# Optimization experiments

Hardware: AMD Instinct MI355X
Metric: run time of the kernel (lower is better)

Reference implementation:

```python
import jax, jax.numpy as jnp
import numpy as np

B, T, V, E, H, K, PAD = 32, 512, 50000, 256, 512, 17, 0


def setup_inputs() -> dict:
    key = jax.random.key(0)
    ks = jax.random.split(key, 16)
    s = 0.05
    input_ids = jax.random.randint(ks[0], (B, T), 1, V)
    lengths = jax.random.randint(ks[1], (B,), T // 2, T + 1)  # >=1 token, mask[:,0] all True
    tags = jax.random.randint(ks[2], (B, T), 0, K)
    mask = jnp.arange(T)[None, :] < lengths[:, None]
    emb = (jax.random.normal(ks[3], (V, E)) * s).at[PAD].set(0.0)  # padding_idx row zeroed
    w_ih_f = jax.random.normal(ks[4], (4 * H, E)) * s
    w_hh_f = jax.random.normal(ks[5], (4 * H, H)) * s
    b_f = jax.random.normal(ks[6], (4 * H,)) * s
    w_ih_b = jax.random.normal(ks[7], (4 * H, E)) * s
    w_hh_b = jax.random.normal(ks[8], (4 * H, H)) * s
    b_b = jax.random.normal(ks[9], (4 * H,)) * s
    w_cls = jax.random.normal(ks[10], (K, 2 * H)) * s
    b_cls = jax.random.normal(ks[11], (K,)) * s
    start_trans = jax.random.normal(ks[12], (K,)) * s
    trans = jax.random.normal(ks[13], (K, K)) * s
    end_trans = jax.random.normal(ks[14], (K,)) * s
    return dict(input_ids=input_ids, lengths=lengths, tags=tags, mask=mask,
                emb=emb, w_ih_f=w_ih_f, w_hh_f=w_hh_f, b_f=b_f,
                w_ih_b=w_ih_b, w_hh_b=w_hh_b, b_b=b_b,
                w_cls=w_cls, b_cls=b_cls,
                start_trans=start_trans, trans=trans, end_trans=end_trans)


def _lstm(xg, w_hh):
    # xg: [B,T,4H] = x @ W_ih^T + b (precomputed); scan adds recurrent term.
    Bq, Hq = xg.shape[0], w_hh.shape[1]

    def step(carry, g_in):
        h, c = carry
        g = g_in + h @ w_hh.T
        i, f, gg, o = jnp.split(g, 4, axis=-1)  # torch gate order i,f,g,o
        c = jax.nn.sigmoid(f) * c + jax.nn.sigmoid(i) * jnp.tanh(gg)
        h = jax.nn.sigmoid(o) * jnp.tanh(c)
        return (h, c), h

    init = (jnp.zeros((Bq, Hq), xg.dtype), jnp.zeros((Bq, Hq), xg.dtype))
    _, hs = jax.lax.scan(step, init, jnp.swapaxes(xg, 0, 1))
    return jnp.swapaxes(hs, 0, 1)  # [B,T,H]


def _forward_math(input_ids, lengths, tags, mask, emb,
                  w_ih_f, w_hh_f, b_f, w_ih_b, w_hh_b, b_b,
                  w_cls, b_cls, start_trans, trans, end_trans):
    x = emb[input_ids]  # [B,T,E]
    # forward direction over padded seq (valid prefix is causally correct)
    hf = _lstm(x @ w_ih_f.T + b_f, w_hh_f)
    # backward direction: reverse each sequence within its own length (packed semantics)
    t = jnp.arange(input_ids.shape[1])[None, :]
    rev = jnp.where(t < lengths[:, None], lengths[:, None] - 1 - t, t)  # involution on valid region
    xr = jnp.take_along_axis(x, rev[:, :, None], axis=1)
    hb = _lstm(xr @ w_ih_b.T + b_b, w_hh_b)
    hb = jnp.take_along_axis(hb, rev[:, :, None], axis=1)
    enc = jnp.concatenate([hf, hb], axis=-1)  # dropout = identity (eval / p=0)
    emissions = enc @ w_cls.T + b_cls  # [B,T,K]
    m = mask.astype(emissions.dtype)
    # ---- CRF numerator (gold path score) ----
    emis_sc = jnp.sum(jnp.take_along_axis(emissions, tags[:, :, None], axis=2)[..., 0] * m, axis=1)
    tr_sc = jnp.sum(trans[tags[:, :-1], tags[:, 1:]] * m[:, 1:], axis=1)
    last_tag = jnp.take_along_axis(tags, (lengths - 1)[:, None], axis=1)[:, 0]
    numer = start_trans[tags[:, 0]] + emis_sc + tr_sc + end_trans[last_tag]
    # ---- CRF partition (forward algorithm) ----
    def fstep(alpha, inp):
        e_t, m_t = inp
        nxt = jax.nn.logsumexp(alpha[:, :, None] + trans[None, :, :] + e_t[:, None, :], axis=1)
        return jnp.where(m_t[:, None], nxt, alpha), None

    alpha0 = start_trans[None, :] + emissions[:, 0]
    alphaT, _ = jax.lax.scan(
        fstep, alpha0,
        (jnp.swapaxes(emissions[:, 1:], 0, 1), jnp.swapaxes(mask[:, 1:], 0, 1)))
    logZ = jax.nn.logsumexp(alphaT + end_trans[None, :], axis=1)
    return -jnp.mean(numer - logZ)  # reduction='mean', negated


def reference(input_ids, lengths, tags, mask, emb, w_ih_f, w_hh_f, b_f,
              w_ih_b, w_hh_b, b_b, w_cls, b_cls, start_trans, trans, end_trans):
    return _forward_math(input_ids, lengths, tags, mask, emb, w_ih_f, w_hh_f, b_f,
                         w_ih_b, w_hh_b, b_b, w_cls, b_cls, start_trans, trans, end_trans)
```

## Files before the change

kernel.cpp:

```cpp
#include <hip/hip_runtime.h>
#include <hip/hip_bf16.h>
#include <stdint.h>

#define B_  32
#define T_  512
#define E_  256
#define H_  512
#define K_  17

typedef unsigned short us;
typedef __attribute__((ext_vector_type(8))) short short8;
typedef __attribute__((ext_vector_type(4))) float f32x4;

__device__ __forceinline__ float bf2f(unsigned int u16) {
    union { unsigned int i; float f; } v; v.i = u16 << 16; return v.f;
}
__device__ __forceinline__ us f2bf(float f) {
    union { float f; unsigned int i; } v; v.f = f;
    unsigned int b = v.i;
    return (us)((b + 0x7FFFu + ((b >> 16) & 1u)) >> 16);
}
__device__ __forceinline__ float sigf(float x) { return 1.0f / (1.0f + __expf(-x)); }
__device__ __forceinline__ float tanhf_(float x) { return 1.0f - 2.0f / (__expf(2.0f * x) + 1.0f); }

__global__ void k_cvt(const float* __restrict__ src, us* __restrict__ dst, int n4) {
    int i = blockIdx.x * 256 + threadIdx.x;
    if (i < n4) {
        float4 v = ((const float4*)src)[i];
        uint2 p;
        p.x = (uint32_t)f2bf(v.x) | ((uint32_t)f2bf(v.y) << 16);
        p.y = (uint32_t)f2bf(v.z) | ((uint32_t)f2bf(v.w) << 16);
        ((uint2*)dst)[i] = p;
    }
}

__global__ void k_init(const int* __restrict__ ids, const int* __restrict__ lengths,
                       int* __restrict__ ids2, int* __restrict__ marker,
                       int* __restrict__ flags, float* __restrict__ out) {
    int idx = blockIdx.x * 256 + threadIdx.x;
    if (idx == 0) { *marker = 1; out[0] = -3328.0f; }
    if (idx < 1024) flags[idx] = 0;
    if (idx < 2 * B_ * T_) {
        int dir = idx >> 14;
        int r   = idx & 16383;
        int t   = r >> 5;
        int b   = r & 31;
        int l   = lengths[b];
        int tt  = (dir == 0) ? t : ((t < l) ? (l - 1 - t) : t);
        ids2[idx] = ids[b * T_ + tt];
    }
}

__launch_bounds__(256)
__global__ void k_xg(const us* __restrict__ emb,
                     const us* __restrict__ wf, const float* __restrict__ bfv,
                     const us* __restrict__ wb, const float* __restrict__ bbv,
                     const int* __restrict__ ids2, us* __restrict__ xg,
                     int* __restrict__ marker) {
    if (blockIdx.x == 0 && blockIdx.y == 0 && blockIdx.z == 0 && threadIdx.x == 0)
        atomicOr(marker, 2);
    int mt = blockIdx.x, nt = blockIdx.y, dir = blockIdx.z;
    const us* W      = dir ? wb  : wf;
    const float* bias = dir ? bbv : bfv;
    const int* id2 = ids2 + dir * (B_ * T_);
    us* xgd = xg + (size_t)dir * B_ * T_ * 2048;
    int m0 = mt * 64, n0 = nt * 64;
    __shared__ __align__(16) us As[64][136];
    __shared__ __align__(16) us Bs[64][136];
    int tid = threadIdx.x;
    int wv = tid >> 6, lane = tid & 63;
    int lm = lane & 15, lg = lane >> 4;
    f32x4 z = {0.f, 0.f, 0.f, 0.f};
    f32x4 acc[4] = {z, z, z, z};
    for (int half = 0; half < 2; ++half) {
        for (int c = tid; c < 1024; c += 256) {
            int row = c >> 4, cb = c & 15;
            int mg = m0 + row;
            int j = mg >> 2, g = mg & 3;
            *(uint4*)&As[row][cb * 8] =
                *(const uint4*)(W + ((size_t)(g * H_ + j)) * E_ + half * 128 + cb * 8);
            int gi = id2[n0 + row];
            *(uint4*)&Bs[row][cb * 8] =
                *(const uint4*)(emb + (size_t)gi * E_ + half * 128 + cb * 8);
        }
        __syncthreads();
#pragma unroll
        for (int kt = 0; kt < 4; ++kt) {
            short8 a = *(const short8*)&As[wv * 16 + lm][kt * 32 + lg * 8];
#pragma unroll
            for (int n2 = 0; n2 < 4; ++n2) {
                short8 b = *(const short8*)&Bs[n2 * 16 + lm][kt * 32 + lg * 8];
                acc[n2] = __builtin_amdgcn_mfma_f32_16x16x32_bf16(a, b, acc[n2], 0, 0, 0);
            }
        }
        __syncthreads();
    }
    int jgb = m0 + wv * 16 + lg * 4;
    int j = jgb >> 2;
#pragma unroll
    for (int n2 = 0; n2 < 4; ++n2) {
        int token = n0 + n2 * 16 + lm;
        us p[4];
#pragma unroll
        for (int q = 0; q < 4; ++q)
            p[q] = f2bf(acc[n2][q] + bias[q * H_ + j]);
        uint2 pv;
        pv.x = (uint32_t)p[0] | ((uint32_t)p[1] << 16);
        pv.y = (uint32_t)p[2] | ((uint32_t)p[3] << 16);
        *(uint2*)(xgd + (size_t)token * 2048 + jgb) = pv;
    }
}

__launch_bounds__(256)
__global__ void k_lstm(const us* __restrict__ whf, const us* __restrict__ whb,
                       const us* __restrict__ xg,
                       us* __restrict__ h_state, us* __restrict__ h_out,
                       int* __restrict__ flags, int* __restrict__ marker) {
    int bid = blockIdx.x;
    int role = bid & 7;
    int tid = threadIdx.x;
    if (bid == 0 && tid == 0) atomicOr(marker, 4);
    if (role >= 2) return;
    int dir = role, w = bid >> 3;
    const us* Wg = dir ? whb : whf;
    __shared__ __align__(16) us Ws[64 * 512];
    __shared__ __align__(4)  us Hx[32 * 16];
    for (int c = tid; c < 4096; c += 256) {
        int row = c >> 6, cb = c & 63;
        int rt = row >> 4, rl = row & 15;
        int jj = rl >> 2, g = rl & 3;
        int srcRow = g * H_ + w * 16 + rt * 4 + jj;
        uint4 v = *(const uint4*)(Wg + (size_t)srcRow * H_ + cb * 8);
        int lb = row * 1024 + ((cb * 16) ^ ((row & 7) << 4));
        *(uint4*)((char*)Ws + lb) = v;
    }
    __syncthreads();
    int wv = tid >> 6, lane = tid & 63;
    int nb = wv & 1, rh = wv >> 1;
    int lm = lane & 15, lg = lane >> 4;
    int b = nb * 16 + lm;
    int jl0 = rh * 8 + lg;
    int jl1 = rh * 8 + 4 + lg;
    const us* xgd = xg + (size_t)dir * B_ * T_ * 2048;
    us* hod = h_out + (size_t)dir * B_ * T_ * H_;
    int* slots = flags + dir * 512;
    const uint64_t* hbase = (const uint64_t*)h_state + (size_t)dir * 8192;
    uint32_t* hw32 = (uint32_t*)h_state + (size_t)dir * 16384;
    float cc0 = 0.f, cc1 = 0.f;
    bool alive = true;
    uint2 vr0 = *(const uint2*)(xgd + ((size_t)b) * 2048 + (w * 16 + jl0) * 4);
    uint2 vr1 = *(const uint2*)(xgd + ((size_t)b) * 2048 + (w * 16 + jl1) * 4);
#pragma unroll 1
    for (int t = 0; t < T_; ++t) {
        f32x4 acc[2];
        if (t > 0) {
            if (wv == 0) {
                int polls = 0;
                for (;;) {
                    int v = (lane < 32)
                        ? __hip_atomic_load(&slots[lane * 16], __ATOMIC_RELAXED, __HIP_MEMORY_SCOPE_AGENT)
                        : 0x7fffffff;
                    if (__all(v >= t) || !alive) break;
                    __builtin_amdgcn_s_sleep(1);
                    if (++polls > 300000) {
                        if (lane == 0) atomicOr(marker, 32);
                        alive = false;
                    }
                }
            }
            __syncthreads();
            const uint64_t* hp = hbase + ((t - 1) & 1) * 4096 + (size_t)b * 128 + lg * 2;
            uint64_t hv[32];
#pragma unroll
            for (int kt = 0; kt < 16; ++kt) {
                hv[2 * kt]     = __hip_atomic_load(hp + kt * 8,     __ATOMIC_RELAXED, __HIP_MEMORY_SCOPE_AGENT);
                hv[2 * kt + 1] = __hip_atomic_load(hp + kt * 8 + 1, __ATOMIC_RELAXED, __HIP_MEMORY_SCOPE_AGENT);
            }
            acc[0][0] = bf2f(vr0.x & 0xffff); acc[0][1] = bf2f(vr0.x >> 16);
            acc[0][2] = bf2f(vr0.y & 0xffff); acc[0][3] = bf2f(vr0.y >> 16);
            acc[1][0] = bf2f(vr1.x & 0xffff); acc[1][1] = bf2f(vr1.x >> 16);
            acc[1][2] = bf2f(vr1.y & 0xffff); acc[1][3] = bf2f(vr1.y >> 16);
#pragma unroll
            for (int ti = 0; ti < 2; ++ti) {
                int r0 = (rh * 2 + ti) * 16 + lm;
                const char* abase = (const char*)Ws + r0 * 1024;
                int sw = (r0 & 7) << 4;
#pragma unroll
                for (int kt = 0; kt < 16; ++kt) {
                    union { uint64_t u[2]; short8 s; } bu;
                    bu.u[0] = hv[2 * kt]; bu.u[1] = hv[2 * kt + 1];
                    short8 a = *(const short8*)(abase + ((kt * 64 + lg * 16) ^ sw));
                    acc[ti] = __builtin_amdgcn_mfma_f32_16x16x32_bf16(a, bu.s, acc[ti], 0, 0, 0);
                }
            }
        } else {
            acc[0][0] = bf2f(vr0.x & 0xffff); acc[0][1] = bf2f(vr0.x >> 16);
            acc[0][2] = bf2f(vr0.y & 0xffff); acc[0][3] = bf2f(vr0.y >> 16);
            acc[1][0] = bf2f(vr1.x & 0xffff); acc[1][1] = bf2f(vr1.x >> 16);
            acc[1][2] = bf2f(vr1.y & 0xffff); acc[1][3] = bf2f(vr1.y >> 16);
        }
        cc0 = sigf(acc[0][1]) * cc0 + sigf(acc[0][0]) * tanhf_(acc[0][2]);
        float h0 = sigf(acc[0][3]) * tanhf_(cc0);
        cc1 = sigf(acc[1][1]) * cc1 + sigf(acc[1][0]) * tanhf_(acc[1][2]);
        float h1 = sigf(acc[1][3]) * tanhf_(cc1);
        us p0 = f2bf(h0), p1 = f2bf(h1);
        Hx[b * 16 + jl0] = p0;
        Hx[b * 16 + jl1] = p1;
        hod[((size_t)b * T_ + t) * H_ + w * 16 + jl0] = p0;
        hod[((size_t)b * T_ + t) * H_ + w * 16 + jl1] = p1;
        __syncthreads();
        {
            uint32_t v = ((const uint32_t*)Hx)[tid];
            int bb = tid >> 3, jp = tid & 7;
            atomicExch(&hw32[(size_t)(t & 1) * 8192 + (size_t)bb * 256 + w * 8 + jp], v);
        }
        __syncthreads();
        if (tid == 0) atomicExch(&slots[w * 16], t + 1);
        if (t + 1 < T_) {
            vr0 = *(const uint2*)(xgd + ((size_t)((t + 1) * 32 + b)) * 2048 + (w * 16 + jl0) * 4);
            vr1 = *(const uint2*)(xgd + ((size_t)((t + 1) * 32 + b)) * 2048 + (w * 16 + jl1) * 4);
        }
    }
}

__launch_bounds__(256)
__global__ void k_emis(const us* __restrict__ h_out,
                       const us* __restrict__ wcls, const float* __restrict__ bcls,
                       const int* __restrict__ lengths, float* __restrict__ emis,
                       int* __restrict__ marker) {
    if (blockIdx.x == 0 && threadIdx.x == 0) atomicOr(marker, 8);
    __shared__ __align__(8) us Wc[17][1032];
    int tid = threadIdx.x;
    for (int c = tid; c < 17 * 256; c += 256) {
        int row = c >> 8; int c4 = (c & 255) * 4;
        *(uint2*)&Wc[row][c4] = *(const uint2*)(wcls + (size_t)row * 1024 + c4);
    }
    __syncthreads();
    int i = blockIdx.x * 8 + (tid >> 5);
    int k = tid & 31;
    int b = i >> 9, t = i & 511;
    int l = lengths[b];
    int trv = (t < l) ? (l - 1 - t) : t;
    const us* hf = h_out + ((size_t)(0 * B_ + b) * T_ + t) * H_;
    const us* hb = h_out + ((size_t)(1 * B_ + b) * T_ + trv) * H_;
    if (k < K_) {
        float acc = bcls[k];
        for (int e = 0; e < H_; e += 4) {
            uint2 hv = *(const uint2*)(hf + e);
            uint2 wv = *(const uint2*)&Wc[k][e];
            acc = fmaf(bf2f(hv.x & 0xffff), bf2f(wv.x & 0xffff), acc);
            acc = fmaf(bf2f(hv.x >> 16),    bf2f(wv.x >> 16),    acc);
            acc = fmaf(bf2f(hv.y & 0xffff), bf2f(wv.y & 0xffff), acc);
            acc = fmaf(bf2f(hv.y >> 16),    bf2f(wv.y >> 16),    acc);
        }
        for (int e = 0; e < H_; e += 4) {
            uint2 hv = *(const uint2*)(hb + e);
            uint2 wv = *(const uint2*)&Wc[k][512 + e];
            acc = fmaf(bf2f(hv.x & 0xffff), bf2f(wv.x & 0xffff), acc);
            acc = fmaf(bf2f(hv.x >> 16),    bf2f(wv.x >> 16),    acc);
            acc = fmaf(bf2f(hv.y & 0xffff), bf2f(wv.y & 0xffff), acc);
            acc = fmaf(bf2f(hv.y >> 16),    bf2f(wv.y >> 16),    acc);
        }
        emis[(size_t)i * 20 + k] = acc;
    }
}

__global__ void k_crf(const float* __restrict__ emis, const int* __restrict__ tags,
                      const int* __restrict__ lengths,
                      const float* __restrict__ start_t, const float* __restrict__ trans_t,
                      const float* __restrict__ end_t, float* __restrict__ res,
                      int* __restrict__ marker) {
    if (blockIdx.x == 0 && threadIdx.x == 0) atomicOr(marker, 16);
    __shared__ float tr[17][18];
    int b = blockIdx.x, tid = threadIdx.x;
    for (int i = tid; i < 289; i += 64) tr[i / 17][i % 17] = trans_t[i];
    __syncthreads();
    int l = lengths[b];
    const int* tg = tags + b * T_;
    const float* eb = emis + (size_t)b * T_ * 20;
    float sn = 0.f;
    for (int t = tid; t < T_; t += 64) {
        if (t < l) {
            sn += eb[t * 20 + tg[t]];
            if (t >= 1) sn += tr[tg[t - 1]][tg[t]];
        }
    }
#pragma unroll
    for (int off = 32; off; off >>= 1) sn += __shfl_xor(sn, off, 64);
    float numer = sn + start_t[tg[0]] + end_t[tg[l - 1]];
    int k = (tid < K_) ? tid : (K_ - 1);
    float trc[17];
#pragma unroll
    for (int j = 0; j < 17; ++j) trc[j] = trans_t[j * 17 + k];
    float alpha = start_t[k] + eb[k];
    for (int t = 1; t < l; ++t) {
        float av[17];
        float m = -1e30f;
#pragma unroll
        for (int j = 0; j < 17; ++j) {
            av[j] = __shfl(alpha, j) + trc[j];
            m = fmaxf(m, av[j]);
        }
        float s = 0.f;
#pragma unroll
        for (int j = 0; j < 17; ++j) s += __expf(av[j] - m);
        alpha = m + __logf(s) + eb[t * 20 + k];
    }
    float v = (tid < K_) ? (alpha + end_t[tid]) : -1e30f;
    float m2 = v;
#pragma unroll
    for (int off = 32; off; off >>= 1) m2 = fmaxf(m2, __shfl_xor(m2, off, 64));
    float s2 = __expf(v - m2);
#pragma unroll
    for (int off = 32; off; off >>= 1) s2 += __shfl_xor(s2, off, 64);
    if (tid == 0) res[b] = numer - (m2 + __logf(s2));
}

__global__ void k_fin(const float* __restrict__ res, int* __restrict__ marker,
                      int hostmask, float* __restrict__ out) {
    int tid = threadIdx.x;
    if (hostmask != 0) {
        if (tid == 0) out[0] = -(16384.0f + 512.0f * (float)hostmask);
        return;
    }
    int dm = atomicOr(marker, 0);
    if (dm != 31) {
        if (tid == 0) out[0] = -(8192.0f + 128.0f * (float)(dm & 63));
        return;
    }
    float v = (tid < B_) ? res[tid] : 0.f;
    unsigned long long nb = __ballot(v != v);
    if (nb != 0ULL) {
        if (tid == 0) out[0] = -(4096.0f + (float)(__ffsll((long long)nb) - 1));
        return;
    }
#pragma unroll
    for (int off = 32; off; off >>= 1) v += __shfl_xor(v, off, 64);
    if (tid == 0) out[0] = -(v / (float)B_);
}

extern "C" void kernel_launch(void* const* d_in, const int* in_sizes, int n_in,
                              void* d_out, int out_size, void* d_ws, size_t ws_size,
                              hipStream_t stream) {
    const int* ids      = (const int*)d_in[0];
    const int* lengths  = (const int*)d_in[1];
    const int* tags     = (const int*)d_in[2];
    const float* emb_f  = (const float*)d_in[4];
    const float* wihf_f = (const float*)d_in[5];
    const float* whhf_f = (const float*)d_in[6];
    const float* bfv    = (const float*)d_in[7];
    const float* wihb_f = (const float*)d_in[8];
    const float* whhb_f = (const float*)d_in[9];
    const float* bbv    = (const float*)d_in[10];
    const float* wcls_f = (const float*)d_in[11];
    const float* bcls   = (const float*)d_in[12];
    const float* start  = (const float*)d_in[13];
    const float* trans  = (const float*)d_in[14];
    const float* endt   = (const float*)d_in[15];
    float* out = (float*)d_out;

    int hm = 0;
    if (n_in != 16 || out_size != 1) hm |= 8;
    const int exp_sz[16] = {
        16384, 32, 16384, 16384,
        12800000,
        524288, 1048576, 2048,
        524288, 1048576, 2048,
        17408, 17,
        17, 289, 17
    };
    if (!(hm & 8))
        for (int i = 0; i < 16; ++i)
            if (in_sizes[i] != exp_sz[i]) hm |= 2;

    char* w = (char*)d_ws;
    size_t off = 0;
    auto carve = [&](size_t bytes) { void* p = w + off; off += (bytes + 255) & ~(size_t)255; return p; };
    int* ids2    = (int*)carve((size_t)2 * B_ * T_ * 4);
    int* marker  = (int*)carve(256);
    int* flags   = (int*)carve(4096);
    float* res   = (float*)carve(256);
    float* emis  = (float*)carve((size_t)B_ * T_ * 20 * 4);
    us* xg       = (us*)carve((size_t)2 * B_ * T_ * 2048 * 2);
    us* h_st     = (us*)carve((size_t)2 * 2 * B_ * H_ * 2);
    us* h_out    = (us*)carve((size_t)2 * B_ * T_ * H_ * 2);
    us* emb_b    = (us*)carve((size_t)12800000 * 2);
    us* wihf_b   = (us*)carve((size_t)524288 * 2);
    us* wihb_b   = (us*)carve((size_t)524288 * 2);
    us* whhf_b   = (us*)carve((size_t)1048576 * 2);
    us* whhb_b   = (us*)carve((size_t)1048576 * 2);
    us* wcls_b   = (us*)carve((size_t)17408 * 2);
    if (off > ws_size) hm |= 4;

    (void)hipGetLastError();
    if ((hm & (2 | 4 | 8)) == 0) {
        k_init<<<(2 * B_ * T_ + 255) / 256, 256, 0, stream>>>(ids, lengths, ids2, marker, flags, out);
        k_cvt<<<(12800000 / 4 + 255) / 256, 256, 0, stream>>>(emb_f,  emb_b,  12800000 / 4);
        k_cvt<<<(524288   / 4 + 255) / 256, 256, 0, stream>>>(wihf_f, wihf_b, 524288 / 4);
        k_cvt<<<(524288   / 4 + 255) / 256, 256, 0, stream>>>(wihb_f, wihb_b, 524288 / 4);
        k_cvt<<<(1048576  / 4 + 255) / 256, 256, 0, stream>>>(whhf_f, whhf_b, 1048576 / 4);
        k_cvt<<<(1048576  / 4 + 255) / 256, 256, 0, stream>>>(whhb_f, whhb_b, 1048576 / 4);
        k_cvt<<<(17408    / 4 + 255) / 256, 256, 0, stream>>>(wcls_f, wcls_b, 17408 / 4);
        k_xg<<<dim3(2048 / 64, B_ * T_ / 64, 2), 256, 0, stream>>>(emb_b, wihf_b, bfv, wihb_b, bbv, ids2, xg, marker);
        k_lstm<<<256, 256, 0, stream>>>(whhf_b, whhb_b, xg, h_st, h_out, flags, marker);
        k_emis<<<B_ * T_ / 8, 256, 0, stream>>>(h_out, wcls_b, bcls, lengths, emis, marker);
        k_crf<<<B_, 64, 0, stream>>>(emis, tags, lengths, start, trans, endt, res, marker);
        if (hipGetLastError() != hipSuccess) hm |= 1;
    }
    k_fin<<<1, 64, 0, stream>>>(res, marker, hm, out);
}
```

Before: 2.890 ms.

## Enlarge xg GEMM tiles and replace LSTM block barrier with per-wave flags

The input-projection GEMM now uses 128x128 tiles, with each wave computing a 4x4 grid of MFMA fragments, to raise data reuse and cut block count. In the recurrent LSTM kernel, each wave now publishes its own ready flag after waiting for its h stores, instead of going through a block-wide barrier and a single thread. Pollers read four flags per lane with 64-bit loads. The h_out stores move after the flag publish so they are off the critical path. This relies on the flag slot spacing (16 ints per w, 4 waves) fitting within each w's region, and on the memory ordering being correct without the barrier.

```diff
diff --git a/kernel.cpp b/kernel.cpp
--- a/kernel.cpp
+++ b/kernel.cpp
@@ -64,16 +64,21 @@
     const float* bias = dir ? bbv : bfv;
     const int* id2 = ids2 + dir * (B_ * T_);
     us* xgd = xg + (size_t)dir * B_ * T_ * 2048;
-    int m0 = mt * 64, n0 = nt * 64;
-    __shared__ __align__(16) us As[64][136];
-    __shared__ __align__(16) us Bs[64][136];
+    int m0 = mt * 128, n0 = nt * 128;
+    __shared__ __align__(16) us As[128][136];
+    __shared__ __align__(16) us Bs[128][136];
     int tid = threadIdx.x;
     int wv = tid >> 6, lane = tid & 63;
+    int wm = wv >> 1, wn = wv & 1;
     int lm = lane & 15, lg = lane >> 4;
     f32x4 z = {0.f, 0.f, 0.f, 0.f};
-    f32x4 acc[4] = {z, z, z, z};
+    f32x4 acc[4][4];
+#pragma unroll
+    for (int i = 0; i < 4; ++i)
+#pragma unroll
+        for (int j = 0; j < 4; ++j) acc[i][j] = z;
     for (int half = 0; half < 2; ++half) {
-        for (int c = tid; c < 1024; c += 256) {
+        for (int c = tid; c < 2048; c += 256) {
             int row = c >> 4, cb = c & 15;
             int mg = m0 + row;
             int j = mg >> 2, g = mg & 3;
@@ -86,28 +91,39 @@
         __syncthreads();
 #pragma unroll
         for (int kt = 0; kt < 4; ++kt) {
-            short8 a = *(const short8*)&As[wv * 16 + lm][kt * 32 + lg * 8];
-#pragma unroll
-            for (int n2 = 0; n2 < 4; ++n2) {
-                short8 b = *(const short8*)&Bs[n2 * 16 + lm][kt * 32 + lg * 8];
-                acc[n2] = __builtin_amdgcn_mfma_f32_16x16x32_bf16(a, b, acc[n2], 0, 0, 0);
+            short8 a[4], b[4];
+#pragma unroll
+            for (int f = 0; f < 4; ++f) {
+                a[f] = *(const short8*)&As[wm * 64 + f * 16 + lm][kt * 32 + lg * 8];
+                b[f] = *(const short8*)&Bs[wn * 64 + f * 16 + lm][kt * 32 + lg * 8];
             }
+#pragma unroll
+            for (int fm = 0; fm < 4; ++fm)
+#pragma unroll
+                for (int fn = 0; fn < 4; ++fn)
+                    acc[fm][fn] = __builtin_amdgcn_mfma_f32_16x16x32_bf16(a[fm], b[fn], acc[fm][fn], 0, 0, 0);
         }
         __syncthreads();
     }
-    int jgb = m0 + wv * 16 + lg * 4;
-    int j = jgb >> 2;
-#pragma unroll
-    for (int n2 = 0; n2 < 4; ++n2) {
-        int token = n0 + n2 * 16 + lm;
-        us p[4];
-#pragma unroll
-        for (int q = 0; q < 4; ++q)
-            p[q] = f2bf(acc[n2][q] + bias[q * H_ + j]);
-        uint2 pv;
-        pv.x = (uint32_t)p[0] | ((uint32_t)p[1] << 16);
-        pv.y = (uint32_t)p[2] | ((uint32_t)p[3] << 16);
-        *(uint2*)(xgd + (size_t)token * 2048 + jgb) = pv;
+#pragma unroll
+    for (int fm = 0; fm < 4; ++fm) {
+        int jgb = m0 + wm * 64 + fm * 16 + lg * 4;
+        int j = jgb >> 2;
+        float bv[4];
+#pragma unroll
+        for (int q = 0; q < 4; ++q) bv[q] = bias[q * H_ + j];
+#pragma unroll
+        for (int fn = 0; fn < 4; ++fn) {
+            int token = n0 + wn * 64 + fn * 16 + lm;
+            us p[4];
+#pragma unroll
+            for (int q = 0; q < 4; ++q)
+                p[q] = f2bf(acc[fm][fn][q] + bv[q]);
+            uint2 pv;
+            pv.x = (uint32_t)p[0] | ((uint32_t)p[1] << 16);
+            pv.y = (uint32_t)p[2] | ((uint32_t)p[3] << 16);
+            *(uint2*)(xgd + (size_t)token * 2048 + jgb) = pv;
+        }
     }
 }
 
@@ -155,12 +171,15 @@
         f32x4 acc[2];
         if (t > 0) {
             if (wv == 0) {
+                const uint64_t* sp = (const uint64_t*)(slots + (lane & 31) * 16);
                 int polls = 0;
                 for (;;) {
-                    int v = (lane < 32)
-                        ? __hip_atomic_load(&slots[lane * 16], __ATOMIC_RELAXED, __HIP_MEMORY_SCOPE_AGENT)
-                        : 0x7fffffff;
-                    if (__all(v >= t) || !alive) break;
+                    uint64_t va = __hip_atomic_load(sp,     __ATOMIC_RELAXED, __HIP_MEMORY_SCOPE_AGENT);
+                    uint64_t vb = __hip_atomic_load(sp + 1, __ATOMIC_RELAXED, __HIP_MEMORY_SCOPE_AGENT);
+                    int s0 = (int)(va & 0xffffffffu), s1 = (int)(va >> 32);
+                    int s2 = (int)(vb & 0xffffffffu), s3 = (int)(vb >> 32);
+                    bool ok = (s0 >= t && s1 >= t && s2 >= t && s3 >= t);
+                    if (__all(ok) || !alive) break;
                     __builtin_amdgcn_s_sleep(1);
                     if (++polls > 300000) {
                         if (lane == 0) atomicOr(marker, 32);
@@ -206,16 +225,18 @@
         us p0 = f2bf(h0), p1 = f2bf(h1);
         Hx[b * 16 + jl0] = p0;
         Hx[b * 16 + jl1] = p1;
-        hod[((size_t)b * T_ + t) * H_ + w * 16 + jl0] = p0;
-        hod[((size_t)b * T_ + t) * H_ + w * 16 + jl1] = p1;
         __syncthreads();
         {
             uint32_t v = ((const uint32_t*)Hx)[tid];
             int bb = tid >> 3, jp = tid & 7;
             atomicExch(&hw32[(size_t)(t & 1) * 8192 + (size_t)bb * 256 + w * 8 + jp], v);
         }
-        __syncthreads();
-        if (tid == 0) atomicExch(&slots[w * 16], t + 1);
+        asm volatile("s_waitcnt vmcnt(0)" ::: "memory");
+        __builtin_amdgcn_sched_barrier(0);
+        if (lane == 0) atomicExch(&slots[w * 16 + wv], t + 1);
+        __builtin_amdgcn_sched_barrier(0);
+        hod[((size_t)b * T_ + t) * H_ + w * 16 + jl0] = p0;
+        hod[((size_t)b * T_ + t) * H_ + w * 16 + jl1] = p1;
         if (t + 1 < T_) {
             vr0 = *(const uint2*)(xgd + ((size_t)((t + 1) * 32 + b)) * 2048 + (w * 16 + jl0) * 4);
             vr1 = *(const uint2*)(xgd + ((size_t)((t + 1) * 32 + b)) * 2048 + (w * 16 + jl1) * 4);
@@ -401,7 +422,7 @@
         k_cvt<<<(1048576  / 4 + 255) / 256, 256, 0, stream>>>(whhf_f, whhf_b, 1048576 / 4);
         k_cvt<<<(1048576  / 4 + 255) / 256, 256, 0, stream>>>(whhb_f, whhb_b, 1048576 / 4);
         k_cvt<<<(17408    / 4 + 255) / 256, 256, 0, stream>>>(wcls_f, wcls_b, 17408 / 4);
-        k_xg<<<dim3(2048 / 64, B_ * T_ / 64, 2), 256, 0, stream>>>(emb_b, wihf_b, bfv, wihb_b, bbv, ids2, xg, marker);
+        k_xg<<<dim3(2048 / 128, B_ * T_ / 128, 2), 256, 0, stream>>>(emb_b, wihf_b, bfv, wihb_b, bbv, ids2, xg, marker);
         k_lstm<<<256, 256, 0, stream>>>(whhf_b, whhb_b, xg, h_st, h_out, flags, marker);
         k_emis<<<B_ * T_ / 8, 256, 0, stream>>>(h_out, wcls_b, bcls, lengths, emis, marker);
         k_crf<<<B_, 64, 0, stream>>>(emis, tags, lengths, start, trans, endt, res, marker);
```

New measurement: 3.117 ms. +7.9%, slower.
